# Optimization experiments

Hardware: AMD Instinct MI355X
Metric: run time of the kernel (lower is better)

## Reference

```python
import jax, jax.numpy as jnp
import numpy as np

N, D = 8192, 512  # scaled from hardcoded 1140, 100


def setup_inputs() -> dict:
    key = jax.random.key(0)
    ks = jax.random.split(key, 7)
    return {
        "U": jax.random.uniform(ks[0], (N, N), jnp.float32),
        "X": jax.random.uniform(ks[1], (N, N), jnp.float32),
        # learned params (torch init was uniform[0,1) for H_1/W0/W1; Linear uses kaiming-ish)
        "H_1": jax.random.uniform(ks[2], (N, D), jnp.float32),
        "W0": jax.random.uniform(ks[3], (N, D), jnp.float32),
        "W1": jax.random.uniform(ks[4], (D, N), jnp.float32),
        "Wa": jax.random.normal(ks[5], (D, N), jnp.float32) * (1.0 / np.sqrt(N)),
        "ba": jnp.zeros((D,), jnp.float32),
    }


def reference(U, X, H_1, W0, W1, Wa, ba):
    # Per-row attention loop, fully vectorized.
    # Note: in the original, att_layer(A2[i]) reads row i BEFORE it is overwritten,
    # so K is computed from the unmodified U (A2 = U / 1).
    K = jnp.tanh(U @ Wa.T + ba)                 # [N, D]  (Linear + Tanh)
    S = jax.nn.softmax(K @ H_1.T, axis=1)       # [N, N]  row i: softmax(H_1 @ K_i)
    S = jax.lax.stop_gradient(S)                # torch: score.detach().numpy() round-trip
    A2 = U * S                                  # [N, N]  elementwise re-weighted rows
    # encoder: nn.Softmax() on 2D input defaults to dim=1
    Z = jax.nn.softmax(A2 @ X @ W0, axis=1)     # [N, D]
    # decoder: Sigmoid
    X_p = jax.nn.sigmoid(U @ Z @ W1)            # [N, N]
    return (X_p, Z)
```

## Files before the change

### kernel.cpp

```cpp
#include <hip/hip_runtime.h>
#include <math.h>


typedef __attribute__((ext_vector_type(8))) short bf16x8;
typedef __attribute__((ext_vector_type(8))) _Float16 f16x8;
typedef __attribute__((ext_vector_type(4))) float f32x4;
typedef __attribute__((ext_vector_type(4))) unsigned short us4;

__device__ __forceinline__ unsigned short f2h(float x) {
    _Float16 h = (_Float16)x;
    return __builtin_bit_cast(unsigned short, h);
}
__device__ __forceinline__ float h2f(unsigned short u) {
    return (float)__builtin_bit_cast(_Float16, u);
}

__device__ __forceinline__ void gload_lds16(const char* g, char* l) {
    __builtin_amdgcn_global_load_lds(
        (const __attribute__((address_space(1))) unsigned int*)g,
        (__attribute__((address_space(3))) unsigned int*)l, 16, 0, 0);
}

__device__ __forceinline__ int swz(int o) {
    return o ^ (((o >> 7) & 7) << 4);
}

__device__ __forceinline__ f32x4 mfma16(bf16x8 a, bf16x8 b, f32x4 c) {
    return __builtin_amdgcn_mfma_f32_16x16x32_f16(
        __builtin_bit_cast(f16x8, a), __builtin_bit_cast(f16x8, b), c, 0, 0, 0);
}

__global__ __launch_bounds__(256)
void convert_f16(const float* __restrict__ in, unsigned short* __restrict__ hi, size_t n)
{
    size_t i = ((size_t)blockIdx.x * blockDim.x + threadIdx.x) * 4;
    const size_t stride = (size_t)gridDim.x * blockDim.x * 4;
    for (; i < n; i += stride) {
        float4 v = *(const float4*)(in + i);
        us4 h;
        h.x = f2h(v.x); h.y = f2h(v.y); h.z = f2h(v.z); h.w = f2h(v.w);
        *(us4*)(hi + i) = h;
    }
}

template<bool CSUB>
__global__ __launch_bounds__(256)
void transpose_cvt(const float* __restrict__ in, unsigned short* __restrict__ hi,
                   const float* __restrict__ cvec, int R, int C)
{
    __shared__ float tile[32][33];
    const int t = threadIdx.x, tx = t & 31, ty = t >> 5;
    const int c0 = blockIdx.x * 32, r0 = blockIdx.y * 32;
#pragma unroll
    for (int i = 0; i < 4; ++i)
        tile[ty + 8 * i][tx] = in[(size_t)(r0 + ty + 8 * i) * C + c0 + tx];
    __syncthreads();
#pragma unroll
    for (int i = 0; i < 4; ++i) {
        const int col = c0 + ty + 8 * i;
        float v = tile[tx][ty + 8 * i];
        if (CSUB) v -= cvec[col];
        hi[(size_t)col * R + r0 + tx] = f2h(v);
    }
}

__global__ __launch_bounds__(256)
void colsum512(const float* __restrict__ in, float* __restrict__ c, int Nrows)
{
    const int t = threadIdx.x;
    const int r0 = blockIdx.x * 16;
    float s0 = 0.f, s1 = 0.f;
    for (int r = 0; r < 16; ++r) {
        const float* row = in + (size_t)(r0 + r) * 512;
        s0 += row[t];
        s1 += row[t + 256];
    }
    atomicAdd(&c[t], s0);
    atomicAdd(&c[t + 256], s1);
}

__global__ void scale_vec(float* __restrict__ c, float s, int n)
{
    const int t = threadIdx.x;
    if (t < n) c[t] *= s;
}

template<int FM, int NPROD, int EPI>
__global__ __launch_bounds__(256)
void gemm_mfma(const unsigned short* __restrict__ Ahi, const unsigned short* __restrict__ Alo,
               const unsigned short* __restrict__ Bh, float* __restrict__ Cf,
               int M, int Ncol, int Kdim)
{
    constexpr int BM = FM * 32;
    constexpr int BN = 128;
    constexpr int ABYTES = BM * 64;
    constexpr int BBYTES = BN * 64;
    constexpr int LDSB = ABYTES * NPROD + BBYTES;
    constexpr int CPW = LDSB / 4096;

    __shared__ __align__(1024) char lds[2][LDSB];

    const int t = threadIdx.x;
    const int w = t >> 6, lane = t & 63;

    const int gx = gridDim.x;
    const int nwg = gx * gridDim.y;
    const int lid = blockIdx.y * gx + blockIdx.x;
    const int tl = (lid & 7) * (nwg >> 3) + (lid >> 3);
    const int m0 = (tl / gx) * BM, n0 = (tl % gx) * BN;

    const int kseg = Kdim / gridDim.z;
    const int kbeg = blockIdx.z * kseg;
    const int ksteps = kseg >> 5;
    const size_t zoff = (size_t)blockIdx.z * ((size_t)M * Ncol);

    const int wr = w >> 1, wc = w & 1;
    const int l15 = lane & 15, kq = lane >> 4;

    const char* gsrc[CPW];
    int lofs[CPW];
#pragma unroll
    for (int c = 0; c < CPW; ++c) {
        const int boff = (w * CPW + c) * 1024;
        lofs[c] = boff;
        const int poff = swz(boff + lane * 16);
        const unsigned short* mat;
        int moff, rbase;
        if (poff < ABYTES)               { mat = Ahi; moff = poff;                   rbase = m0; }
        else if (poff < ABYTES + BBYTES) { mat = Bh;  moff = poff - ABYTES;          rbase = n0; }
        else                             { mat = Alo; moff = poff - ABYTES - BBYTES; rbase = m0; }
        gsrc[c] = (const char*)(mat + (size_t)(rbase + (moff >> 6)) * Kdim + kbeg) + (moff & 63);
    }

    int aoffS[FM], aloS[FM], boffS[4];
#pragma unroll
    for (int m = 0; m < FM; ++m) {
        const int o = (wr * (FM * 16) + m * 16 + l15) * 64 + kq * 16;
        aoffS[m] = swz(o);
        aloS[m] = swz(ABYTES + BBYTES + o);
    }
#pragma unroll
    for (int n = 0; n < 4; ++n)
        boffS[n] = swz(ABYTES + (wc * 64 + n * 16 + l15) * 64 + kq * 16);

    f32x4 acc[FM][4];
#pragma unroll
    for (int m = 0; m < FM; ++m)
#pragma unroll
        for (int n = 0; n < 4; ++n)
            acc[m][n] = (f32x4)(0.f);

    auto stage = [&](int buf) {
#pragma unroll
        for (int c = 0; c < CPW; ++c) {
            gload_lds16(gsrc[c], &lds[buf][lofs[c]]);
            gsrc[c] += 64;
        }
    };

    stage(0);
    __syncthreads();

    int cur = 0;
    for (int ks = 0; ks < ksteps; ++ks) {
        if (ks + 1 < ksteps) stage(cur ^ 1);

        const char* Lb = lds[cur];
        bf16x8 ah[FM], al[FM], bb[4];
#pragma unroll
        for (int m = 0; m < FM; ++m) {
            ah[m] = *(const bf16x8*)(Lb + aoffS[m]);
            if constexpr (NPROD == 2)
                al[m] = *(const bf16x8*)(Lb + aloS[m]);
        }
#pragma unroll
        for (int n = 0; n < 4; ++n)
            bb[n] = *(const bf16x8*)(Lb + boffS[n]);

        __builtin_amdgcn_s_setprio(1);
#pragma unroll
        for (int n = 0; n < 4; ++n)
#pragma unroll
            for (int m = 0; m < FM; ++m)
                acc[m][n] = mfma16(ah[m], bb[n], acc[m][n]);
        if constexpr (NPROD == 2) {
#pragma unroll
            for (int n = 0; n < 4; ++n)
#pragma unroll
                for (int m = 0; m < FM; ++m)
                    acc[m][n] = mfma16(al[m], bb[n], acc[m][n]);
        }
        __builtin_amdgcn_s_setprio(0);

        __syncthreads();
        cur ^= 1;
    }

#pragma unroll
    for (int m = 0; m < FM; ++m) {
        const int rowb = m0 + wr * (FM * 16) + m * 16 + kq * 4;
#pragma unroll
        for (int n = 0; n < 4; ++n) {
            const int col = n0 + wc * 64 + n * 16 + l15;
#pragma unroll
            for (int r = 0; r < 4; ++r) {
                float v = acc[m][n][r];
                const size_t idx = (size_t)(rowb + r) * Ncol + col;
                if constexpr (EPI == 0) {
                    Cf[zoff + idx] = v;
                } else {
                    Cf[idx] = 1.f / (1.f + __expf(-v));
                }
            }
        }
    }
}

template<int RED>
__global__ __launch_bounds__(256)
void reduce_splitk(const float* __restrict__ P, size_t seg,
                   const float* __restrict__ ba, const float* __restrict__ rs,
                   const float* __restrict__ cv, float scale, int Ncol,
                   float* __restrict__ outf, unsigned short* __restrict__ outh)
{
    const size_t i = ((size_t)blockIdx.x * blockDim.x + threadIdx.x) * 4;
    float4 a = *(const float4*)(P + i);
    float4 b = *(const float4*)(P + seg + i);
    float4 c = *(const float4*)(P + 2 * seg + i);
    float4 d = *(const float4*)(P + 3 * seg + i);
    float s0 = a.x + b.x + c.x + d.x;
    float s1 = a.y + b.y + c.y + d.y;
    float s2 = a.z + b.z + c.z + d.z;
    float s3 = a.w + b.w + c.w + d.w;
    const int col = (int)(i % (size_t)Ncol);

    if constexpr (RED == 0) {
        us4 h;
        h.x = f2h(tanhf(s0 + ba[col + 0]));
        h.y = f2h(tanhf(s1 + ba[col + 1]));
        h.z = f2h(tanhf(s2 + ba[col + 2]));
        h.w = f2h(tanhf(s3 + ba[col + 3]));
        *(us4*)(outh + i) = h;
    } else if constexpr (RED == 1) {
        float4 o; o.x = s0; o.y = s1; o.z = s2; o.w = s3;
        *(float4*)(outf + i) = o;
    } else if constexpr (RED == 2) {
        const float rsr = rs[i / (size_t)Ncol];
        float4 o;
        o.x = s0 * scale + rsr * cv[col + 0];
        o.y = s1 * scale + rsr * cv[col + 1];
        o.z = s2 * scale + rsr * cv[col + 2];
        o.w = s3 * scale + rsr * cv[col + 3];
        *(float4*)(outf + i) = o;
    } else {
        us4 h;
        h.x = f2h(s0); h.y = f2h(s1); h.z = f2h(s2); h.w = f2h(s3);
        *(us4*)(outh + i) = h;
    }
}

__device__ inline float blockReduceMax(float v, float* sred)
{
    for (int o = 32; o > 0; o >>= 1) v = fmaxf(v, __shfl_down(v, o));
    const int lane = threadIdx.x & 63, wid = threadIdx.x >> 6;
    if (lane == 0) sred[wid] = v;
    __syncthreads();
    if (threadIdx.x == 0) {
        float m = sred[0];
        for (int w = 1; w < 4; ++w) m = fmaxf(m, sred[w]);
        sred[0] = m;
    }
    __syncthreads();
    float r = sred[0];
    __syncthreads();
    return r;
}

__device__ inline float blockReduceSum(float v, float* sred)
{
    for (int o = 32; o > 0; o >>= 1) v += __shfl_down(v, o);
    const int lane = threadIdx.x & 63, wid = threadIdx.x >> 6;
    if (lane == 0) sred[wid] = v;
    __syncthreads();
    if (threadIdx.x == 0) {
        float m = sred[0];
        for (int w = 1; w < 4; ++w) m += sred[w];
        sred[0] = m;
    }
    __syncthreads();
    float r = sred[0];
    __syncthreads();
    return r;
}

__global__ __launch_bounds__(256)
void softmax_mul_f16s(const float* __restrict__ Lrow, const unsigned short* __restrict__ Uh,
                      unsigned short* __restrict__ hi, float* __restrict__ rowsum, int Ncols)
{
    __shared__ float srow[8192];
    __shared__ float sred[8];
    const int t = threadIdx.x;
    const size_t base = (size_t)blockIdx.x * Ncols;

    float lmax = -3.402823466e38f;
    for (int c = t * 4; c < Ncols; c += 1024) {
        float4 v = *(const float4*)(Lrow + base + c);
        *(float4*)&srow[c] = v;
        lmax = fmaxf(lmax, fmaxf(fmaxf(v.x, v.y), fmaxf(v.z, v.w)));
    }
    const float rmax = blockReduceMax(lmax, sred);

    float lsum = 0.f;
    for (int c = t * 4; c < Ncols; c += 1024) {
        float4 v = *(float4*)&srow[c];
        v.x = __expf(v.x - rmax);
        v.y = __expf(v.y - rmax);
        v.z = __expf(v.z - rmax);
        v.w = __expf(v.w - rmax);
        *(float4*)&srow[c] = v;
        lsum += v.x + v.y + v.z + v.w;
    }
    const float rsum = blockReduceSum(lsum, sred);
    const float inv = 1.f / rsum;

    float a2sum = 0.f;
    for (int c = t * 4; c < Ncols; c += 1024) {
        float4 e = *(float4*)&srow[c];
        us4 u = *(const us4*)(Uh + base + c);
        float a0 = h2f(u.x) * e.x * inv, a1 = h2f(u.y) * e.y * inv;
        float a2 = h2f(u.z) * e.z * inv, a3 = h2f(u.w) * e.w * inv;
        a2sum += a0 + a1 + a2 + a3;
        us4 h;
        h.x = f2h(a0 * 1024.f);
        h.y = f2h(a1 * 1024.f);
        h.z = f2h(a2 * 1024.f);
        h.w = f2h(a3 * 1024.f);
        *(us4*)(hi + base + c) = h;
    }
    const float rssum = blockReduceSum(a2sum, sred);
    if (t == 0) rowsum[blockIdx.x] = rssum;
}

__global__ __launch_bounds__(256)
void softmax_inplace_small(float* buf, int D)
{
    __shared__ float sred[8];
    const int t = threadIdx.x;
    const size_t base = (size_t)blockIdx.x * D;
    float2 v = *(float2*)(buf + base + t * 2);
    const float rmax = blockReduceMax(fmaxf(v.x, v.y), sred);
    const float e0 = __expf(v.x - rmax);
    const float e1 = __expf(v.y - rmax);
    const float rsum = blockReduceSum(e0 + e1, sred);
    const float inv = 1.f / rsum;
    float2 o;
    o.x = e0 * inv;
    o.y = e1 * inv;
    *(float2*)(buf + base + t * 2) = o;
}

template<int EPI, bool TB>
__global__ __launch_bounds__(256)
void gemm_f32(const float* __restrict__ A, const float* __restrict__ B,
              const float* __restrict__ bias, float* __restrict__ C,
              int M, int Ncol, int Kdim)
{
    constexpr int FBM = 128, FBN = 128, FBK = 8;
    __shared__ float As[FBK][FBM];
    __shared__ float Bs[FBK][FBN];
    const int t  = threadIdx.x;
    const int tx = t & 15, ty = t >> 4;
    const int m0 = blockIdx.y * FBM, n0 = blockIdx.x * FBN;

    const int arow  = t >> 1;
    const int acol4 = (t & 1) * 4;
    const int brow  = t >> 5;
    const int bcol4 = (t & 31) * 4;

    float acc[8][8];
#pragma unroll
    for (int i = 0; i < 8; ++i)
#pragma unroll
        for (int j = 0; j < 8; ++j) acc[i][j] = 0.f;

    const float* Aptr = A + (size_t)(m0 + arow) * Kdim + acol4;
    const float* Bptr;
    if (TB) Bptr = B + (size_t)(n0 + arow) * Kdim + acol4;
    else    Bptr = B + (size_t)brow * Ncol + n0 + bcol4;

    float4 av = *(const float4*)(Aptr);
    float4 bv = *(const float4*)(Bptr);

    for (int k0 = 0; k0 < Kdim; k0 += FBK) {
        As[acol4 + 0][arow] = av.x;
        As[acol4 + 1][arow] = av.y;
        As[acol4 + 2][arow] = av.z;
        As[acol4 + 3][arow] = av.w;
        if (TB) {
            Bs[acol4 + 0][arow] = bv.x;
            Bs[acol4 + 1][arow] = bv.y;
            Bs[acol4 + 2][arow] = bv.z;
            Bs[acol4 + 3][arow] = bv.w;
        } else {
            *(float4*)&Bs[brow][bcol4] = bv;
        }
        __syncthreads();

        if (k0 + FBK < Kdim) {
            av = *(const float4*)(Aptr + (k0 + FBK));
            if (TB) bv = *(const float4*)(Bptr + (k0 + FBK));
            else    bv = *(const float4*)(Bptr + (size_t)(k0 + FBK) * Ncol);
        }

#pragma unroll
        for (int kk = 0; kk < FBK; ++kk) {
            float a[8], b[8];
            *(float4*)&a[0] = *(const float4*)&As[kk][ty * 4];
            *(float4*)&a[4] = *(const float4*)&As[kk][64 + ty * 4];
            *(float4*)&b[0] = *(const float4*)&Bs[kk][tx * 4];
            *(float4*)&b[4] = *(const float4*)&Bs[kk][64 + tx * 4];
#pragma unroll
            for (int i = 0; i < 8; ++i)
#pragma unroll
                for (int j = 0; j < 8; ++j)
                    acc[i][j] = fmaf(a[i], b[j], acc[i][j]);
        }
        __syncthreads();
    }

#pragma unroll
    for (int ib = 0; ib < 2; ++ib) {
#pragma unroll
        for (int ii = 0; ii < 4; ++ii) {
            const int i = ib * 4 + ii;
            const size_t row = (size_t)(m0 + ib * 64 + ty * 4 + ii);
            float* crow = C + row * (size_t)Ncol;
#pragma unroll
            for (int jb = 0; jb < 2; ++jb) {
                const int col0 = n0 + jb * 64 + tx * 4;
                float4 v;
                v.x = acc[i][jb * 4 + 0];
                v.y = acc[i][jb * 4 + 1];
                v.z = acc[i][jb * 4 + 2];
                v.w = acc[i][jb * 4 + 3];
                if (EPI == 1) {
                    v.x = tanhf(v.x + bias[col0 + 0]);
                    v.y = tanhf(v.y + bias[col0 + 1]);
                    v.z = tanhf(v.z + bias[col0 + 2]);
                    v.w = tanhf(v.w + bias[col0 + 3]);
                } else if (EPI == 2) {
                    v.x = 1.f / (1.f + __expf(-v.x));
                    v.y = 1.f / (1.f + __expf(-v.y));
                    v.z = 1.f / (1.f + __expf(-v.z));
                    v.w = 1.f / (1.f + __expf(-v.w));
                }
                *(float4*)(crow + col0) = v;
            }
        }
    }
}

__global__ __launch_bounds__(256)
void softmax_mul_f32(float* buf, const float* __restrict__ U, int Ncols)
{
    __shared__ float srow[8192];
    __shared__ float sred[8];
    const int t = threadIdx.x;
    const size_t base = (size_t)blockIdx.x * Ncols;

    float lmax = -3.402823466e38f;
    for (int c = t * 4; c < Ncols; c += 1024) {
        float4 v = *(const float4*)(buf + base + c);
        *(float4*)&srow[c] = v;
        lmax = fmaxf(lmax, fmaxf(fmaxf(v.x, v.y), fmaxf(v.z, v.w)));
    }
    const float rmax = blockReduceMax(lmax, sred);

    float lsum = 0.f;
    for (int c = t * 4; c < Ncols; c += 1024) {
        float4 v = *(float4*)&srow[c];
        v.x = __expf(v.x - rmax);
        v.y = __expf(v.y - rmax);
        v.z = __expf(v.z - rmax);
        v.w = __expf(v.w - rmax);
        *(float4*)&srow[c] = v;
        lsum += v.x + v.y + v.z + v.w;
    }
    const float rsum = blockReduceSum(lsum, sred);
    const float inv = 1.f / rsum;

    for (int c = t * 4; c < Ncols; c += 1024) {
        float4 e = *(float4*)&srow[c];
        float4 u = *(const float4*)(U + base + c);
        float4 o;
        o.x = u.x * e.x * inv;
        o.y = u.y * e.y * inv;
        o.z = u.z * e.z * inv;
        o.w = u.w * e.w * inv;
        *(float4*)(buf + base + c) = o;
    }
}

extern "C" void kernel_launch(void* const* d_in, const int* in_sizes, int n_in,
                              void* d_out, int out_size, void* d_ws, size_t ws_size,
                              hipStream_t stream)
{
    const float* U  = (const float*)d_in[0];
    const float* X  = (const float*)d_in[1];
    const float* H1 = (const float*)d_in[2];
    const float* W0 = (const float*)d_in[3];
    const float* W1 = (const float*)d_in[4];
    const float* Wa = (const float*)d_in[5];
    const float* ba = (const float*)d_in[6];
    const int D = in_sizes[6];
    const int N = (int)((long long)in_sizes[2] / D);
    const size_t NN = (size_t)N * N, ND = (size_t)N * D;

    float* Xp = (float*)d_out;
    float* Zp = Xp + NN;

    char* p = (char*)d_ws;
    auto alloc = [&](size_t bytes) { char* r = p; p += (bytes + 255) & ~(size_t)255; return r; };
    unsigned short* wa_h  = (unsigned short*)alloc(ND * 2);
    unsigned short* h1_h  = (unsigned short*)alloc(ND * 2);
    unsigned short* k_h   = (unsigned short*)alloc(ND * 2);
    unsigned short* w0t_h = (unsigned short*)alloc(ND * 2);
    unsigned short* vbt   = (unsigned short*)alloc(ND * 2);
    unsigned short* zt_h  = (unsigned short*)alloc(ND * 2);
    unsigned short* uz_h  = (unsigned short*)alloc(ND * 2);
    unsigned short* w1t_h = (unsigned short*)alloc(ND * 2);
    float*          xw0f  = (float*)alloc(ND * 4);
    float*          cvec  = (float*)alloc((size_t)D * 4);
    float*          rsum  = (float*)alloc((size_t)N * 4);
    float*          Pp    = (float*)alloc(ND * 4 * 4);
    unsigned short* Uh    = (unsigned short*)alloc(NN * 2);
    unsigned short* Xh    = (unsigned short*)alloc(NN * 2);
    const size_t need = (size_t)(p - (char*)d_ws);

    dim3 blk(256);

    if (N == 8192 && D == 512 && ws_size >= need) {
        const dim3 gSlimK(D / 128, N / 128, 4);
        const dim3 gBig(N / 128, N / 128);
        const dim3 gT(D / 32, N / 32);
        const dim3 gTw1(N / 32, D / 32);
        const dim3 gRed((unsigned)(ND / 1024));
        const int cgrid = 4096;
        const unsigned short* nullu = nullptr;
        unsigned short* nullw = nullptr;
        const float* nullf = nullptr;

        hipLaunchKernelGGL(convert_f16, dim3(cgrid), blk, 0, stream, U, Uh, NN);
        hipLaunchKernelGGL(convert_f16, dim3(1024), blk, 0, stream, Wa, wa_h, ND);
        hipLaunchKernelGGL((gemm_mfma<4, 1, 0>), gSlimK, blk, 0, stream,
                           Uh, nullu, wa_h, Pp, N, D, N);
        hipLaunchKernelGGL((reduce_splitk<0>), gRed, blk, 0, stream,
                           Pp, ND, ba, nullf, nullf, 0.f, D, (float*)nullptr, k_h);
        hipLaunchKernelGGL(convert_f16, dim3(1024), blk, 0, stream, H1, h1_h, ND);
        hipLaunchKernelGGL((gemm_mfma<4, 1, 0>), gBig, blk, 0, stream,
                           k_h, nullu, h1_h, Xp, N, N, D);
        hipLaunchKernelGGL(convert_f16, dim3(cgrid), blk, 0, stream, X, Xh, NN);
        hipLaunchKernelGGL((transpose_cvt<false>), gT, blk, 0, stream, W0, w0t_h, nullf, N, D);
        hipLaunchKernelGGL((gemm_mfma<4, 1, 0>), gSlimK, blk, 0, stream,
                           Xh, nullu, w0t_h, Pp, N, D, N);
        hipLaunchKernelGGL((reduce_splitk<1>), gRed, blk, 0, stream,
                           Pp, ND, nullf, nullf, nullf, 0.f, D, xw0f, nullw);
        hipMemsetAsync(cvec, 0, (size_t)D * 4, stream);
        hipLaunchKernelGGL(colsum512, dim3(N / 16), blk, 0, stream, xw0f, cvec, N);
        hipLaunchKernelGGL(scale_vec, dim3(1), dim3(512), 0, stream, cvec, 1.0f / (float)N, D);
        hipLaunchKernelGGL((transpose_cvt<true>), gT, blk, 0, stream, xw0f, vbt, cvec, N, D);
        hipLaunchKernelGGL(softmax_mul_f16s, dim3(N), blk, 0, stream, Xp, Uh, Xh, rsum, N);
        hipLaunchKernelGGL((gemm_mfma<4, 1, 0>), gSlimK, blk, 0, stream,
                           Xh, nullu, vbt, Pp, N, D, N);
        hipLaunchKernelGGL((reduce_splitk<2>), gRed, blk, 0, stream,
                           Pp, ND, nullf, rsum, cvec, 1.0f / 1024.f, D, Zp, nullw);
        hipLaunchKernelGGL(softmax_inplace_small, dim3(N), blk, 0, stream, Zp, D);
        hipLaunchKernelGGL((transpose_cvt<false>), gT, blk, 0, stream, Zp, zt_h, nullf, N, D);
        hipLaunchKernelGGL((gemm_mfma<4, 1, 0>), gSlimK, blk, 0, stream,
                           Uh, nullu, zt_h, Pp, N, D, N);
        hipLaunchKernelGGL((reduce_splitk<3>), gRed, blk, 0, stream,
                           Pp, ND, nullf, nullf, nullf, 0.f, D, (float*)nullptr, uz_h);
        hipLaunchKernelGGL((transpose_cvt<false>), gTw1, blk, 0, stream, W1, w1t_h, nullf, D, N);
        hipLaunchKernelGGL((gemm_mfma<4, 1, 2>), gBig, blk, 0, stream,
                           uz_h, nullu, w1t_h, Xp, N, N, D);
    } else {
        float* bufA = (float*)d_ws;
        dim3 gD(D / 128, N / 128);
        dim3 gN(N / 128, N / 128);
        hipLaunchKernelGGL((gemm_f32<1, true>),  gD, blk, 0, stream, U,    Wa, ba,      bufA, N, D, N);
        hipLaunchKernelGGL((gemm_f32<0, true>),  gN, blk, 0, stream, bufA, H1, nullptr, Xp,   N, N, D);
        hipLaunchKernelGGL(softmax_mul_f32, dim3(N), blk, 0, stream, Xp, U, N);
        hipLaunchKernelGGL((gemm_f32<0, false>), gD, blk, 0, stream, X,    W0, nullptr, bufA, N, D, N);
        hipLaunchKernelGGL((gemm_f32<0, false>), gD, blk, 0, stream, Xp,   bufA, nullptr, Zp, N, D, N);
        hipLaunchKernelGGL(softmax_inplace_small, dim3(N), blk, 0, stream, Zp, D);
        hipLaunchKernelGGL((gemm_f32<0, false>), gD, blk, 0, stream, U,    Zp, nullptr, bufA, N, D, N);
        hipLaunchKernelGGL((gemm_f32<2, false>), gN, blk, 0, stream, bufA, W1, nullptr, Xp,  N, N, D);
    }
}
```

Measured before the change: 1.085 ms.

## Store logits as fp16, widen big GEMM tiles, fuse Z softmax with transpose

The logits GEMM K@H1^T now writes fp16 directly, halving the N×N intermediate that the softmax-multiply kernel reads. The two big N×N GEMMs use a 512-thread 128×256 tile. The Z softmax is fused with the transpose-to-fp16 into one kernel. The unused lo-split (NPROD) path is removed. Storing logits in fp16 loses some precision before the softmax, and the larger tile changes occupancy and register pressure.

```diff
diff --git a/kernel.cpp b/kernel.cpp
--- a/kernel.cpp
+++ b/kernel.cpp
@@ -85,18 +85,20 @@
     if (t < n) c[t] *= s;
 }
 
-template<int FM, int NPROD, int EPI>
-__global__ __launch_bounds__(256)
-void gemm_mfma(const unsigned short* __restrict__ Ahi, const unsigned short* __restrict__ Alo,
+template<int FM, int WM, int WN, int EPI>
+__global__ __launch_bounds__(WM * WN * 64)
+void gemm_mfma(const unsigned short* __restrict__ Ahi,
                const unsigned short* __restrict__ Bh, float* __restrict__ Cf,
+               unsigned short* __restrict__ Ch,
                int M, int Ncol, int Kdim)
 {
-    constexpr int BM = FM * 32;
-    constexpr int BN = 128;
+    constexpr int NWAVES = WM * WN;
+    constexpr int BM = WM * FM * 16;
+    constexpr int BN = WN * 64;
     constexpr int ABYTES = BM * 64;
     constexpr int BBYTES = BN * 64;
-    constexpr int LDSB = ABYTES * NPROD + BBYTES;
-    constexpr int CPW = LDSB / 4096;
+    constexpr int LDSB = ABYTES + BBYTES;
+    constexpr int CPW = LDSB / 1024 / NWAVES;
 
     __shared__ __align__(1024) char lds[2][LDSB];
 
@@ -114,7 +116,7 @@
     const int ksteps = kseg >> 5;
     const size_t zoff = (size_t)blockIdx.z * ((size_t)M * Ncol);
 
-    const int wr = w >> 1, wc = w & 1;
+    const int wr = w / WN, wc = w % WN;
     const int l15 = lane & 15, kq = lane >> 4;
 
     const char* gsrc[CPW];
@@ -126,19 +128,15 @@
         const int poff = swz(boff + lane * 16);
         const unsigned short* mat;
         int moff, rbase;
-        if (poff < ABYTES)               { mat = Ahi; moff = poff;                   rbase = m0; }
-        else if (poff < ABYTES + BBYTES) { mat = Bh;  moff = poff - ABYTES;          rbase = n0; }
-        else                             { mat = Alo; moff = poff - ABYTES - BBYTES; rbase = m0; }
+        if (poff < ABYTES) { mat = Ahi; moff = poff;          rbase = m0; }
+        else               { mat = Bh;  moff = poff - ABYTES; rbase = n0; }
         gsrc[c] = (const char*)(mat + (size_t)(rbase + (moff >> 6)) * Kdim + kbeg) + (moff & 63);
     }
 
-    int aoffS[FM], aloS[FM], boffS[4];
-#pragma unroll
-    for (int m = 0; m < FM; ++m) {
-        const int o = (wr * (FM * 16) + m * 16 + l15) * 64 + kq * 16;
-        aoffS[m] = swz(o);
-        aloS[m] = swz(ABYTES + BBYTES + o);
-    }
+    int aoffS[FM], boffS[4];
+#pragma unroll
+    for (int m = 0; m < FM; ++m)
+        aoffS[m] = swz((wr * (FM * 16) + m * 16 + l15) * 64 + kq * 16);
 #pragma unroll
     for (int n = 0; n < 4; ++n)
         boffS[n] = swz(ABYTES + (wc * 64 + n * 16 + l15) * 64 + kq * 16);
@@ -166,13 +164,10 @@
         if (ks + 1 < ksteps) stage(cur ^ 1);
 
         const char* Lb = lds[cur];
-        bf16x8 ah[FM], al[FM], bb[4];
-#pragma unroll
-        for (int m = 0; m < FM; ++m) {
+        bf16x8 ah[FM], bb[4];
+#pragma unroll
+        for (int m = 0; m < FM; ++m)
             ah[m] = *(const bf16x8*)(Lb + aoffS[m]);
-            if constexpr (NPROD == 2)
-                al[m] = *(const bf16x8*)(Lb + aloS[m]);
-        }
 #pragma unroll
         for (int n = 0; n < 4; ++n)
             bb[n] = *(const bf16x8*)(Lb + boffS[n]);
@@ -183,13 +178,6 @@
 #pragma unroll
             for (int m = 0; m < FM; ++m)
                 acc[m][n] = mfma16(ah[m], bb[n], acc[m][n]);
-        if constexpr (NPROD == 2) {
-#pragma unroll
-            for (int n = 0; n < 4; ++n)
-#pragma unroll
-                for (int m = 0; m < FM; ++m)
-                    acc[m][n] = mfma16(al[m], bb[n], acc[m][n]);
-        }
         __builtin_amdgcn_s_setprio(0);
 
         __syncthreads();
@@ -208,8 +196,10 @@
                 const size_t idx = (size_t)(rowb + r) * Ncol + col;
                 if constexpr (EPI == 0) {
                     Cf[zoff + idx] = v;
+                } else if constexpr (EPI == 2) {
+                    Cf[idx] = 1.f / (1.f + __expf(-v));
                 } else {
-                    Cf[idx] = 1.f / (1.f + __expf(-v));
+                    Ch[idx] = f2h(v);
                 }
             }
         }
@@ -294,7 +284,8 @@
 }
 
 __global__ __launch_bounds__(256)
-void softmax_mul_f16s(const float* __restrict__ Lrow, const unsigned short* __restrict__ Uh,
+void softmax_mul_f16s(const unsigned short* __restrict__ Lrow,
+                      const unsigned short* __restrict__ Uh,
                       unsigned short* __restrict__ hi, float* __restrict__ rowsum, int Ncols)
 {
     __shared__ float srow[8192];
@@ -304,7 +295,9 @@
 
     float lmax = -3.402823466e38f;
     for (int c = t * 4; c < Ncols; c += 1024) {
-        float4 v = *(const float4*)(Lrow + base + c);
+        us4 lv = *(const us4*)(Lrow + base + c);
+        float4 v;
+        v.x = h2f(lv.x); v.y = h2f(lv.y); v.z = h2f(lv.z); v.w = h2f(lv.w);
         *(float4*)&srow[c] = v;
         lmax = fmaxf(lmax, fmaxf(fmaxf(v.x, v.y), fmaxf(v.z, v.w)));
     }
@@ -339,6 +332,63 @@
     }
     const float rssum = blockReduceSum(a2sum, sred);
     if (t == 0) rowsum[blockIdx.x] = rssum;
+}
+
+__global__ __launch_bounds__(256)
+void softmax16_t(float* __restrict__ buf, unsigned short* __restrict__ zt, int N)
+{
+    __shared__ float s[16][513];
+    const int t = threadIdx.x, lane = t & 63, wid = t >> 6;
+    const int r0 = blockIdx.x * 16;
+
+#pragma unroll
+    for (int i = 0; i < 8; ++i) {
+        const int flat = i * 256 + t;
+        const int row = flat >> 7;
+        const int c4 = (flat & 127) * 4;
+        float4 v = *(const float4*)(buf + (size_t)(r0 + row) * 512 + c4);
+        s[row][c4 + 0] = v.x; s[row][c4 + 1] = v.y;
+        s[row][c4 + 2] = v.z; s[row][c4 + 3] = v.w;
+    }
+    __syncthreads();
+
+#pragma unroll
+    for (int rr = 0; rr < 4; ++rr) {
+        const int row = wid * 4 + rr;
+        float vals[8];
+        float m = -3.402823466e38f;
+#pragma unroll
+        for (int j = 0; j < 8; ++j) { vals[j] = s[row][lane * 8 + j]; m = fmaxf(m, vals[j]); }
+#pragma unroll
+        for (int o = 32; o > 0; o >>= 1) m = fmaxf(m, __shfl_xor(m, o));
+        float sum = 0.f;
+#pragma unroll
+        for (int j = 0; j < 8; ++j) { vals[j] = __expf(vals[j] - m); sum += vals[j]; }
+#pragma unroll
+        for (int o = 32; o > 0; o >>= 1) sum += __shfl_xor(sum, o);
+        const float inv = 1.f / sum;
+        float4 o1, o2;
+        o1.x = vals[0] * inv; o1.y = vals[1] * inv; o1.z = vals[2] * inv; o1.w = vals[3] * inv;
+        o2.x = vals[4] * inv; o2.y = vals[5] * inv; o2.z = vals[6] * inv; o2.w = vals[7] * inv;
+        s[row][lane * 8 + 0] = o1.x; s[row][lane * 8 + 1] = o1.y;
+        s[row][lane * 8 + 2] = o1.z; s[row][lane * 8 + 3] = o1.w;
+        s[row][lane * 8 + 4] = o2.x; s[row][lane * 8 + 5] = o2.y;
+        s[row][lane * 8 + 6] = o2.z; s[row][lane * 8 + 7] = o2.w;
+        *(float4*)(buf + (size_t)(r0 + row) * 512 + lane * 8) = o1;
+        *(float4*)(buf + (size_t)(r0 + row) * 512 + lane * 8 + 4) = o2;
+    }
+    __syncthreads();
+
+#pragma unroll
+    for (int cc = 0; cc < 2; ++cc) {
+        const int col = t * 2 + cc;
+        unsigned short tmp[16];
+#pragma unroll
+        for (int row = 0; row < 16; ++row) tmp[row] = f2h(s[row][col]);
+#pragma unroll
+        for (int q = 0; q < 4; ++q)
+            *(us4*)(zt + (size_t)col * N + r0 + q * 4) = *(us4*)&tmp[q * 4];
+    }
 }
 
 __global__ __launch_bounds__(256)
@@ -537,52 +587,51 @@
     unsigned short* Xh    = (unsigned short*)alloc(NN * 2);
     const size_t need = (size_t)(p - (char*)d_ws);
 
-    dim3 blk(256);
+    dim3 blk(256), blk512(512);
 
     if (N == 8192 && D == 512 && ws_size >= need) {
+        unsigned short* Lh = (unsigned short*)Xp;
         const dim3 gSlimK(D / 128, N / 128, 4);
-        const dim3 gBig(N / 128, N / 128);
+        const dim3 gBig(N / 256, N / 128);
         const dim3 gT(D / 32, N / 32);
         const dim3 gTw1(N / 32, D / 32);
         const dim3 gRed((unsigned)(ND / 1024));
         const int cgrid = 4096;
-        const unsigned short* nullu = nullptr;
         unsigned short* nullw = nullptr;
         const float* nullf = nullptr;
 
         hipLaunchKernelGGL(convert_f16, dim3(cgrid), blk, 0, stream, U, Uh, NN);
         hipLaunchKernelGGL(convert_f16, dim3(1024), blk, 0, stream, Wa, wa_h, ND);
-        hipLaunchKernelGGL((gemm_mfma<4, 1, 0>), gSlimK, blk, 0, stream,
-                           Uh, nullu, wa_h, Pp, N, D, N);
+        hipLaunchKernelGGL((gemm_mfma<4, 2, 2, 0>), gSlimK, blk, 0, stream,
+                           Uh, wa_h, Pp, nullw, N, D, N);
         hipLaunchKernelGGL((reduce_splitk<0>), gRed, blk, 0, stream,
                            Pp, ND, ba, nullf, nullf, 0.f, D, (float*)nullptr, k_h);
         hipLaunchKernelGGL(convert_f16, dim3(1024), blk, 0, stream, H1, h1_h, ND);
-        hipLaunchKernelGGL((gemm_mfma<4, 1, 0>), gBig, blk, 0, stream,
-                           k_h, nullu, h1_h, Xp, N, N, D);
+        hipLaunchKernelGGL((gemm_mfma<4, 2, 4, 3>), gBig, blk512, 0, stream,
+                           k_h, h1_h, (float*)nullptr, Lh, N, N, D);
         hipLaunchKernelGGL(convert_f16, dim3(cgrid), blk, 0, stream, X, Xh, NN);
         hipLaunchKernelGGL((transpose_cvt<false>), gT, blk, 0, stream, W0, w0t_h, nullf, N, D);
-        hipLaunchKernelGGL((gemm_mfma<4, 1, 0>), gSlimK, blk, 0, stream,
-                           Xh, nullu, w0t_h, Pp, N, D, N);
+        hipLaunchKernelGGL((gemm_mfma<4, 2, 2, 0>), gSlimK, blk, 0, stream,
+                           Xh, w0t_h, Pp, nullw, N, D, N);
         hipLaunchKernelGGL((reduce_splitk<1>), gRed, blk, 0, stream,
                            Pp, ND, nullf, nullf, nullf, 0.f, D, xw0f, nullw);
         hipMemsetAsync(cvec, 0, (size_t)D * 4, stream);
         hipLaunchKernelGGL(colsum512, dim3(N / 16), blk, 0, stream, xw0f, cvec, N);
         hipLaunchKernelGGL(scale_vec, dim3(1), dim3(512), 0, stream, cvec, 1.0f / (float)N, D);
         hipLaunchKernelGGL((transpose_cvt<true>), gT, blk, 0, stream, xw0f, vbt, cvec, N, D);
-        hipLaunchKernelGGL(softmax_mul_f16s, dim3(N), blk, 0, stream, Xp, Uh, Xh, rsum, N);
-        hipLaunchKernelGGL((gemm_mfma<4, 1, 0>), gSlimK, blk, 0, stream,
-                           Xh, nullu, vbt, Pp, N, D, N);
+        hipLaunchKernelGGL(softmax_mul_f16s, dim3(N), blk, 0, stream, Lh, Uh, Xh, rsum, N);
+        hipLaunchKernelGGL((gemm_mfma<4, 2, 2, 0>), gSlimK, blk, 0, stream,
+                           Xh, vbt, Pp, nullw, N, D, N);
         hipLaunchKernelGGL((reduce_splitk<2>), gRed, blk, 0, stream,
                            Pp, ND, nullf, rsum, cvec, 1.0f / 1024.f, D, Zp, nullw);
-        hipLaunchKernelGGL(softmax_inplace_small, dim3(N), blk, 0, stream, Zp, D);
-        hipLaunchKernelGGL((transpose_cvt<false>), gT, blk, 0, stream, Zp, zt_h, nullf, N, D);
-        hipLaunchKernelGGL((gemm_mfma<4, 1, 0>), gSlimK, blk, 0, stream,
-                           Uh, nullu, zt_h, Pp, N, D, N);
+        hipLaunchKernelGGL(softmax16_t, dim3(N / 16), blk, 0, stream, Zp, zt_h, N);
+        hipLaunchKernelGGL((gemm_mfma<4, 2, 2, 0>), gSlimK, blk, 0, stream,
+                           Uh, zt_h, Pp, nullw, N, D, N);
         hipLaunchKernelGGL((reduce_splitk<3>), gRed, blk, 0, stream,
                            Pp, ND, nullf, nullf, nullf, 0.f, D, (float*)nullptr, uz_h);
         hipLaunchKernelGGL((transpose_cvt<false>), gTw1, blk, 0, stream, W1, w1t_h, nullf, D, N);
-        hipLaunchKernelGGL((gemm_mfma<4, 1, 2>), gBig, blk, 0, stream,
-                           uz_h, nullu, w1t_h, Xp, N, N, D);
+        hipLaunchKernelGGL((gemm_mfma<4, 2, 4, 2>), gBig, blk512, 0, stream,
+                           uz_h, w1t_h, Xp, nullw, N, N, D);
     } else {
         float* bufA = (float*)d_ws;
         dim3 gD(D / 128, N / 128);
```

After: 1.029 ms. 1.05x faster.
